# Kernel tuning notes

Measured on AMD Instinct MI355X. Metric: run time of the kernel, lower is better.

The kernel has to match this reference:

```python
import jax, jax.numpy as jnp
import numpy as np

MAX_DISP = 4          # displacement radius -> 9x9 = 81 output channels
B, C, H, W = 8, 128, 96, 160


def setup_inputs() -> dict:
    key = jax.random.key(0)
    k1, k2 = jax.random.split(key)
    tensorFirst = jax.random.normal(k1, (B, C, H, W), dtype=jnp.float32)
    tensorSecond = jax.random.normal(k2, (B, C, H, W), dtype=jnp.float32)
    return {"tensorFirst": tensorFirst, "tensorSecond": tensorSecond}


def correlation(first, second):
    # first, second: [B, C, H, W]
    b, c, h, w = first.shape
    d = MAX_DISP
    pad = jnp.pad(second, ((0, 0), (0, 0), (d, d), (d, d)))  # [B,C,H+8,W+8]
    inv_c = jnp.asarray(1.0 / c, dtype=first.dtype)
    # channel order: (dy+4)*9 + (dx+4), dx fastest (matches CUDA kernel)
    chans = [
        (first * pad[:, :, dy:dy + h, dx:dx + w]).sum(axis=1) * inv_c
        for dy in range(2 * d + 1)
        for dx in range(2 * d + 1)
    ]
    return jnp.stack(chans, axis=1)  # [B, 81, H, W]


def reference(tensorFirst, tensorSecond):
    return correlation(tensorFirst, tensorSecond)
```

## Files before the change

### kernel.cpp

```cpp
#include <hip/hip_runtime.h>
#include <stdint.h>


typedef __attribute__((ext_vector_type(8))) short bf16x8;
typedef __attribute__((ext_vector_type(4))) float f32x4;

constexpr int Bn = 8, Cn = 128, Hn = 96, Wn = 160;
constexpr int CHS = Hn * Wn;

__device__ __forceinline__ uint32_t bf16rne(float f) {
    uint32_t u = __float_as_uint(f);
    return (u + 0x7FFFu + ((u >> 16) & 1u)) >> 16;
}
__device__ __forceinline__ uint32_t pk(float a, float b) {
    return bf16rne(a) | (bf16rne(b) << 16);
}

__global__ __launch_bounds__(1024)
void corrfused(const float* __restrict__ first, const float* __restrict__ second,
               float* __restrict__ out)
{
    __shared__ uint4 smem[16 * 48 * 4];

    const int tid  = threadIdx.x;
    const int w    = tid >> 6;
    const int lane = tid & 63;
    const int quad = lane >> 4;
    const int n16  = lane & 15;
    const int s    = w & 1;
    const int r    = w >> 1;
    const int x0   = blockIdx.x * 32;
    const int y0   = blockIdx.y * 8;
    const int b    = blockIdx.z;
    const int y    = y0 + r;
    const int x0s  = x0 + 16 * s;

    bf16x8 aF[4];
    {
        const float* fp = first + (size_t)b * Cn * CHS + (size_t)y * Wn + x0s + n16;
        #pragma unroll
        for (int kc = 0; kc < 4; ++kc) {
            float f[8];
            #pragma unroll
            for (int j = 0; j < 8; ++j)
                f[j] = fp[(size_t)(32 * kc + 8 * quad + j) * CHS];
            union { uint32_t u[4]; bf16x8 v; } cv;
            cv.u[0] = pk(f[0], f[1]); cv.u[1] = pk(f[2], f[3]);
            cv.u[2] = pk(f[4], f[5]); cv.u[3] = pk(f[6], f[7]);
            aF[kc] = cv.v;
        }
    }

    const float* sb = second + (size_t)b * Cn * CHS;
    int goff[3], lpos[3];
    bool val[3];
    #pragma unroll
    for (int i = 0; i < 3; ++i) {
        int e = tid + i * 1024;
        int row = e / 192, rem = e % 192;
        int xw = rem >> 2, q = rem & 3;
        int gy = y0 + row - 4, gx = x0 + xw - 8;
        val[i]  = (gy >= 0) && (gy < Hn) && (gx >= 0) && (gx < Wn);
        goff[i] = val[i] ? (8 * q * CHS + gy * Wn + gx) : 0;
        lpos[i] = (row * 48 + xw) * 4 + ((q + xw + (xw >> 2)) & 3);
    }

    int bo[2];
    #pragma unroll
    for (int t = 0; t < 2; ++t) {
        int xwr = 16 * (s + t) + n16;
        bo[t] = xwr * 4 + ((quad + xwr + (xwr >> 2)) & 3);
    }

    f32x4 acc[9][2];
    #pragma unroll
    for (int dy = 0; dy < 9; ++dy)
        #pragma unroll
        for (int t = 0; t < 2; ++t)
            acc[dy][t] = (f32x4){0.f, 0.f, 0.f, 0.f};

    float fr[3][8];
    #pragma unroll
    for (int i = 0; i < 3; ++i)
        #pragma unroll
        for (int j = 0; j < 8; ++j)
            fr[i][j] = sb[goff[i] + (size_t)j * CHS];

    #pragma unroll
    for (int kc = 0; kc < 4; ++kc) {
        #pragma unroll
        for (int i = 0; i < 3; ++i) {
            uint4 o;
            o.x = pk(fr[i][0], fr[i][1]); o.y = pk(fr[i][2], fr[i][3]);
            o.z = pk(fr[i][4], fr[i][5]); o.w = pk(fr[i][6], fr[i][7]);
            if (!val[i]) o = make_uint4(0u, 0u, 0u, 0u);
            smem[lpos[i]] = o;
        }
        __syncthreads();
        if (kc < 3) {
            #pragma unroll
            for (int i = 0; i < 3; ++i)
                #pragma unroll
                for (int j = 0; j < 8; ++j)
                    fr[i][j] = sb[goff[i] + (size_t)(32 * (kc + 1) + j) * CHS];
        }
        #pragma unroll
        for (int dy = 0; dy < 9; ++dy) {
            const int rb = (r + dy) * 192;
            #pragma unroll
            for (int t = 0; t < 2; ++t) {
                union { uint4 u; bf16x8 v; } bf;
                bf.u = smem[rb + bo[t]];
                acc[dy][t] = __builtin_amdgcn_mfma_f32_16x16x32_bf16(
                                 aF[kc], bf.v, acc[dy][t], 0, 0, 0);
            }
        }
        __syncthreads();
    }

    const float inv = 1.0f / 128.0f;
    float* sm = (float*)smem;
    float* ob = out + (size_t)b * 81 * CHS + (size_t)y * Wn + x0s;
    const int wb = w * 540;
    #pragma unroll
    for (int ck = 0; ck < 3; ++ck) {
        #pragma unroll
        for (int d = 0; d < 3; ++d)
            #pragma unroll
            for (int t = 0; t < 2; ++t)
                #pragma unroll
                for (int reg = 0; reg < 4; ++reg) {
                    int mm  = quad * 4 + reg;
                    int dxc = 16 * t + n16 - mm - 4;
                    if (dxc >= 0 && dxc <= 8)
                        sm[wb + (d * 9 + dxc) * 20 + mm] = acc[ck * 3 + d][t][reg] * inv;
                }
        __syncthreads();
        #pragma unroll
        for (int ii = 0; ii < 2; ++ii) {
            int slot = lane + ii * 64;
            if (slot < 108) {
                int chn = slot >> 2, g = slot & 3;
                float4 v = *(const float4*)&sm[wb + chn * 20 + 4 * g];
                int ch = (ck * 3 + chn / 9) * 9 + chn % 9;
                *(float4*)(ob + (size_t)ch * CHS + 4 * g) = v;
            }
        }
        __syncthreads();
    }
}

extern "C" void kernel_launch(void* const* d_in, const int* in_sizes, int n_in,
                              void* d_out, int out_size, void* d_ws, size_t ws_size,
                              hipStream_t stream) {
    (void)in_sizes; (void)n_in; (void)d_ws; (void)ws_size; (void)out_size;
    const float* first  = (const float*)d_in[0];
    const float* second = (const float*)d_in[1];
    float* out = (float*)d_out;
    corrfused<<<dim3(Wn / 32, Hn / 8, Bn), dim3(1024, 1, 1), 0, stream>>>(
        first, second, out);
}
```

Baseline: 204.4 us.

## Halve block tile to 16 columns, remap blocks by batch, stream first-tensor loads

The block tile shrinks from 32x8 pixels with 1024 threads to 16x8 pixels with 512 threads, and launch bounds now request 4 blocks per CU. The shared halo becomes 32 columns wide. Block indices are remapped so consecutive blocks come from different batches. First-tensor fragments are now loaded per channel chunk inside the loop instead of all up front, which cuts register pressure. The cost is more halo redundancy per output pixel (32 loaded columns for 16 outputs instead of 48 for 32), so second-tensor traffic rises.

```diff
diff --git a/kernel.cpp b/kernel.cpp
--- a/kernel.cpp
+++ b/kernel.cpp
@@ -16,61 +16,50 @@
     return bf16rne(a) | (bf16rne(b) << 16);
 }
 
-__global__ __launch_bounds__(1024)
+__global__ __launch_bounds__(512, 4)
 void corrfused(const float* __restrict__ first, const float* __restrict__ second,
                float* __restrict__ out)
 {
-    __shared__ uint4 smem[16 * 48 * 4];
+    __shared__ uint4 smem[16 * 32 * 4];
 
     const int tid  = threadIdx.x;
     const int w    = tid >> 6;
     const int lane = tid & 63;
     const int quad = lane >> 4;
     const int n16  = lane & 15;
-    const int s    = w & 1;
-    const int r    = w >> 1;
-    const int x0   = blockIdx.x * 32;
-    const int y0   = blockIdx.y * 8;
-    const int b    = blockIdx.z;
+    const int r    = w;
+
+    const int d    = (int)blockIdx.x + 10 * ((int)blockIdx.y + 12 * (int)blockIdx.z);
+    const int tile = (d & 7) * 120 + (d >> 3);
+    const int b    = tile / 120;
+    const int rem  = tile % 120;
+    const int y0   = (rem / 10) * 8;
+    const int x0   = (rem % 10) * 16;
     const int y    = y0 + r;
-    const int x0s  = x0 + 16 * s;
-
-    bf16x8 aF[4];
-    {
-        const float* fp = first + (size_t)b * Cn * CHS + (size_t)y * Wn + x0s + n16;
-        #pragma unroll
-        for (int kc = 0; kc < 4; ++kc) {
-            float f[8];
-            #pragma unroll
-            for (int j = 0; j < 8; ++j)
-                f[j] = fp[(size_t)(32 * kc + 8 * quad + j) * CHS];
-            union { uint32_t u[4]; bf16x8 v; } cv;
-            cv.u[0] = pk(f[0], f[1]); cv.u[1] = pk(f[2], f[3]);
-            cv.u[2] = pk(f[4], f[5]); cv.u[3] = pk(f[6], f[7]);
-            aF[kc] = cv.v;
-        }
-    }
 
     const float* sb = second + (size_t)b * Cn * CHS;
-    int goff[3], lpos[3];
-    bool val[3];
+    int goff[4], lpos[4];
+    bool val[4];
     #pragma unroll
-    for (int i = 0; i < 3; ++i) {
-        int e = tid + i * 1024;
-        int row = e / 192, rem = e % 192;
-        int xw = rem >> 2, q = rem & 3;
-        int gy = y0 + row - 4, gx = x0 + xw - 8;
+    for (int i = 0; i < 4; ++i) {
+        int e   = tid + i * 512;
+        int row = e >> 7;
+        int xw  = (e >> 2) & 31;
+        int q   = e & 3;
+        int gy  = y0 + row - 4, gx = x0 + xw - 8;
         val[i]  = (gy >= 0) && (gy < Hn) && (gx >= 0) && (gx < Wn);
         goff[i] = val[i] ? (8 * q * CHS + gy * Wn + gx) : 0;
-        lpos[i] = (row * 48 + xw) * 4 + ((q + xw + (xw >> 2)) & 3);
+        lpos[i] = (row * 32 + xw) * 4 + ((q + xw + (xw >> 2)) & 3);
     }
 
     int bo[2];
     #pragma unroll
     for (int t = 0; t < 2; ++t) {
-        int xwr = 16 * (s + t) + n16;
+        int xwr = 16 * t + n16;
         bo[t] = xwr * 4 + ((quad + xwr + (xwr >> 2)) & 3);
     }
+
+    const float* fp = first + (size_t)b * Cn * CHS + (size_t)y * Wn + x0 + n16;
 
     f32x4 acc[9][2];
     #pragma unroll
@@ -79,40 +68,64 @@
         for (int t = 0; t < 2; ++t)
             acc[dy][t] = (f32x4){0.f, 0.f, 0.f, 0.f};
 
-    float fr[3][8];
+    float f0[2][8];
     #pragma unroll
-    for (int i = 0; i < 3; ++i)
+    for (int i = 0; i < 2; ++i)
         #pragma unroll
         for (int j = 0; j < 8; ++j)
-            fr[i][j] = sb[goff[i] + (size_t)j * CHS];
+            f0[i][j] = sb[goff[i] + (size_t)j * CHS];
 
     #pragma unroll
     for (int kc = 0; kc < 4; ++kc) {
         #pragma unroll
-        for (int i = 0; i < 3; ++i) {
+        for (int i = 0; i < 2; ++i) {
             uint4 o;
-            o.x = pk(fr[i][0], fr[i][1]); o.y = pk(fr[i][2], fr[i][3]);
-            o.z = pk(fr[i][4], fr[i][5]); o.w = pk(fr[i][6], fr[i][7]);
+            o.x = pk(f0[i][0], f0[i][1]); o.y = pk(f0[i][2], f0[i][3]);
+            o.z = pk(f0[i][4], f0[i][5]); o.w = pk(f0[i][6], f0[i][7]);
             if (!val[i]) o = make_uint4(0u, 0u, 0u, 0u);
             smem[lpos[i]] = o;
+        }
+        float f1[2][8], fa[8];
+        #pragma unroll
+        for (int i = 0; i < 2; ++i)
+            #pragma unroll
+            for (int j = 0; j < 8; ++j)
+                f1[i][j] = sb[goff[2 + i] + (size_t)(32 * kc + j) * CHS];
+        #pragma unroll
+        for (int j = 0; j < 8; ++j)
+            fa[j] = fp[(size_t)(32 * kc + 8 * quad + j) * CHS];
+        #pragma unroll
+        for (int i = 0; i < 2; ++i) {
+            uint4 o;
+            o.x = pk(f1[i][0], f1[i][1]); o.y = pk(f1[i][2], f1[i][3]);
+            o.z = pk(f1[i][4], f1[i][5]); o.w = pk(f1[i][6], f1[i][7]);
+            if (!val[2 + i]) o = make_uint4(0u, 0u, 0u, 0u);
+            smem[lpos[2 + i]] = o;
+        }
+        bf16x8 aF;
+        {
+            union { uint32_t u[4]; bf16x8 v; } cv;
+            cv.u[0] = pk(fa[0], fa[1]); cv.u[1] = pk(fa[2], fa[3]);
+            cv.u[2] = pk(fa[4], fa[5]); cv.u[3] = pk(fa[6], fa[7]);
+            aF = cv.v;
         }
         __syncthreads();
         if (kc < 3) {
             #pragma unroll
-            for (int i = 0; i < 3; ++i)
+            for (int i = 0; i < 2; ++i)
                 #pragma unroll
                 for (int j = 0; j < 8; ++j)
-                    fr[i][j] = sb[goff[i] + (size_t)(32 * (kc + 1) + j) * CHS];
+                    f0[i][j] = sb[goff[i] + (size_t)(32 * (kc + 1) + j) * CHS];
         }
         #pragma unroll
         for (int dy = 0; dy < 9; ++dy) {
-            const int rb = (r + dy) * 192;
+            const int rb = (r + dy) * 128;
             #pragma unroll
             for (int t = 0; t < 2; ++t) {
                 union { uint4 u; bf16x8 v; } bf;
                 bf.u = smem[rb + bo[t]];
                 acc[dy][t] = __builtin_amdgcn_mfma_f32_16x16x32_bf16(
-                                 aF[kc], bf.v, acc[dy][t], 0, 0, 0);
+                                 aF, bf.v, acc[dy][t], 0, 0, 0);
             }
         }
         __syncthreads();
@@ -120,12 +133,12 @@
 
     const float inv = 1.0f / 128.0f;
     float* sm = (float*)smem;
-    float* ob = out + (size_t)b * 81 * CHS + (size_t)y * Wn + x0s;
+    float* ob = out + (size_t)b * 81 * CHS + (size_t)y * Wn + x0;
     const int wb = w * 540;
     #pragma unroll
     for (int ck = 0; ck < 3; ++ck) {
         #pragma unroll
-        for (int d = 0; d < 3; ++d)
+        for (int dd = 0; dd < 3; ++dd)
             #pragma unroll
             for (int t = 0; t < 2; ++t)
                 #pragma unroll
@@ -133,7 +146,7 @@
                     int mm  = quad * 4 + reg;
                     int dxc = 16 * t + n16 - mm - 4;
                     if (dxc >= 0 && dxc <= 8)
-                        sm[wb + (d * 9 + dxc) * 20 + mm] = acc[ck * 3 + d][t][reg] * inv;
+                        sm[wb + (dd * 9 + dxc) * 20 + mm] = acc[ck * 3 + dd][t][reg] * inv;
                 }
         __syncthreads();
         #pragma unroll
@@ -157,6 +170,6 @@
     const float* first  = (const float*)d_in[0];
     const float* second = (const float*)d_in[1];
     float* out = (float*)d_out;
-    corrfused<<<dim3(Wn / 32, Hn / 8, Bn), dim3(1024, 1, 1), 0, stream>>>(
+    corrfused<<<dim3(Wn / 16, Hn / 8, Bn), dim3(512, 1, 1), 0, stream>>>(
         first, second, out);
 }
```

New measurement: 182.2 us. 10.9% less time.
